# Kernel tuning notes

Measured on AMD Instinct MI355X. Metric: run time of the kernel, lower is better.

Reference implementation:

```python
import jax, jax.numpy as jnp
import numpy as np

B, N, C, H = 32, 4096, 768, 8
DH = C // H

def setup_inputs() -> dict:
    key = jax.random.key(0)
    k1, k2, k3, k4, k5, k6 = jax.random.split(key, 6)
    s = 0.02
    return {
        "x": jax.random.normal(k1, (B, N, C), dtype=jnp.float32),
        "queries": jax.random.normal(k2, (C,), dtype=jnp.float32),
        "Wq": jax.random.normal(k3, (C, C), dtype=jnp.float32) * s,
        "Wkv": jax.random.normal(k4, (2 * C, C), dtype=jnp.float32) * s,
        "Wproj": jax.random.normal(k5, (C, C), dtype=jnp.float32) * s,
        "bproj": jax.random.normal(k6, (C,), dtype=jnp.float32) * s,
    }

def reference(x, queries, Wq, Wkv, Wproj, bproj):
    # q: single learnable query, shared across batch. torch Linear: y = x @ W^T
    q = (queries @ Wq.T).reshape(H, DH)              # [H, DH]
    kv = jnp.einsum('bnc,ec->bne', x, Wkv)           # [B, N, 2C]
    k, v = jnp.split(kv, 2, axis=-1)
    k = k.reshape(B, N, H, DH)
    v = v.reshape(B, N, H, DH)
    # NOTE: original applies no 1/sqrt(d) scaling
    dots = jnp.einsum('hd,bnhd->bhn', q, k)          # [B, H, N]
    attn = jax.nn.softmax(dots, axis=-1)
    out = jnp.einsum('bhn,bnhd->bhd', attn, v)       # [B, H, DH]
    out = out.reshape(B, 1, C)
    out = jnp.einsum('bnc,ec->bne', out, Wproj) + bproj
    return out                                        # [B, 1, C]
```

## Files before the change

kernel.cpp:

```cpp
#include <hip/hip_runtime.h>

#define B_ 32
#define N_ 4096
#define C_ 768
#define H_ 8
#define DH_ 96
#define TILE 8
#define ROWS 256
#define NT (ROWS / TILE)
#define NCH (N_ / ROWS)
#define TFL (TILE * C_)
#define NDG 4

struct F3 { float x, y, z; };

#define BARL() do { asm volatile("s_waitcnt lgkmcnt(0)" ::: "memory"); \
                    __builtin_amdgcn_s_barrier(); } while (0)

__global__ __launch_bounds__(256) void k_prep(const float* __restrict__ queries,
    const float* __restrict__ Wq, const float* __restrict__ Wkv,
    float* __restrict__ wqep) {
  __shared__ float qh[24];
  const int h = blockIdx.x, dg = blockIdx.y;
  const int tid = threadIdx.x, lane = tid & 63, wv = tid >> 6;
  const int d0 = dg * 24;

  float4 q0 = *(const float4*)(queries + lane * 4);
  float4 q1 = *(const float4*)(queries + 256 + lane * 4);
  float4 q2 = *(const float4*)(queries + 512 + lane * 4);
#pragma unroll
  for (int j = 0; j < 6; ++j) {
    int dl = wv * 6 + j;
    const float* wr = Wq + (size_t)(h * DH_ + d0 + dl) * C_ + lane * 4;
    float4 w0 = *(const float4*)(wr);
    float4 w1 = *(const float4*)(wr + 256);
    float4 w2 = *(const float4*)(wr + 512);
    float a = w0.x * q0.x;
    a = fmaf(w0.y, q0.y, a); a = fmaf(w0.z, q0.z, a); a = fmaf(w0.w, q0.w, a);
    a = fmaf(w1.x, q1.x, a); a = fmaf(w1.y, q1.y, a);
    a = fmaf(w1.z, q1.z, a); a = fmaf(w1.w, q1.w, a);
    a = fmaf(w2.x, q2.x, a); a = fmaf(w2.y, q2.y, a);
    a = fmaf(w2.z, q2.z, a); a = fmaf(w2.w, q2.w, a);
#pragma unroll
    for (int off = 32; off; off >>= 1) a += __shfl_xor(a, off);
    if (lane == 0) qh[dl] = a;
  }
  __syncthreads();

  const int c0 = tid * 3;
  const float* base = Wkv + (size_t)(h * DH_ + d0) * C_ + c0;
  float a0 = 0.f, a1 = 0.f, a2 = 0.f;
#pragma unroll 8
  for (int d = 0; d < 24; ++d) {
    float qd = qh[d];
    const float* p = base + (size_t)d * C_;
    a0 = fmaf(qd, p[0], a0);
    a1 = fmaf(qd, p[1], a1);
    a2 = fmaf(qd, p[2], a2);
  }
  float* o = wqep + ((size_t)dg * H_ + h) * C_ + c0;
  o[0] = a0; o[1] = a1; o[2] = a2;
}

__global__ __attribute__((amdgpu_flat_work_group_size(256, 256),
                          amdgpu_waves_per_eu(2, 2))) void k_fused(
    const float* __restrict__ x, const float* __restrict__ wqep,
    float* __restrict__ part, float* __restrict__ sout) {
  extern __shared__ __align__(16) float xdyn[];
  __shared__ __align__(16) float wlds[2][TILE][H_];
  __shared__ float sden[4][4];

  const int ch = blockIdx.x, b = blockIdx.y;
  const int tid = threadIdx.x, lane = tid & 63, wid = tid >> 6;
  const int rbase = (wid & 1) * 4;
  const int hbase = (wid >> 1) * 4;
  const int col = lane * 4;
  const float* xc = x + ((size_t)b * N_ + (size_t)ch * ROWS) * C_;

  float4 wqv[4][3];
#pragma unroll
  for (int h = 0; h < 4; ++h)
#pragma unroll
    for (int p = 0; p < 3; ++p) {
      float4 s = *(const float4*)(wqep + (size_t)(hbase + h) * C_ + p * 256 + col);
#pragma unroll
      for (int dg = 1; dg < NDG; ++dg) {
        float4 v = *(const float4*)(wqep + ((size_t)dg * H_ + hbase + h) * C_ + p * 256 + col);
        s.x += v.x; s.y += v.y; s.z += v.z; s.w += v.w;
      }
      wqv[h][p] = s;
    }

  float acc[H_][3];
#pragma unroll
  for (int h = 0; h < H_; ++h) { acc[h][0] = 0.f; acc[h][1] = 0.f; acc[h][2] = 0.f; }
  float sreg = 0.f;

#define STAGE(BI, T) do {                                                      \
    const float* gt_ = xc + (size_t)(T) * TFL;                                 \
    float* bn_ = xdyn + (size_t)(BI) * TFL;                                    \
    _Pragma("unroll")                                                          \
    for (int j = 0; j < 6; ++j) {                                              \
      int k = wid * 6 + j;                                                     \
      __builtin_amdgcn_global_load_lds(                                        \
        (const __attribute__((address_space(1))) void*)(gt_ + k * 256 + lane * 4), \
        (__attribute__((address_space(3))) void*)(bn_ + k * 256),              \
        16, 0, 0);                                                             \
    }                                                                          \
  } while (0)

#define PHASEC(XB, PC) do {                                                    \
    const int c0 = tid * 3;                                                    \
    _Pragma("unroll")                                                          \
    for (int r = 0; r < TILE; ++r) {                                           \
      float4 wA = *(const float4*)(&wlds[PC][r][0]);                           \
      float4 wB = *(const float4*)(&wlds[PC][r][4]);                           \
      F3 xv = *(const F3*)((XB) + (size_t)r * C_ + c0);                        \
      acc[0][0] = fmaf(wA.x, xv.x, acc[0][0]);                                 \
      acc[0][1] = fmaf(wA.x, xv.y, acc[0][1]);                                 \
      acc[0][2] = fmaf(wA.x, xv.z, acc[0][2]);                                 \
      acc[1][0] = fmaf(wA.y, xv.x, acc[1][0]);                                 \
      acc[1][1] = fmaf(wA.y, xv.y, acc[1][1]);                                 \
      acc[1][2] = fmaf(wA.y, xv.z, acc[1][2]);                                 \
      acc[2][0] = fmaf(wA.z, xv.x, acc[2][0]);                                 \
      acc[2][1] = fmaf(wA.z, xv.y, acc[2][1]);                                 \
      acc[2][2] = fmaf(wA.z, xv.z, acc[2][2]);                                 \
      acc[3][0] = fmaf(wA.w, xv.x, acc[3][0]);                                 \
      acc[3][1] = fmaf(wA.w, xv.y, acc[3][1]);                                 \
      acc[3][2] = fmaf(wA.w, xv.z, acc[3][2]);                                 \
      acc[4][0] = fmaf(wB.x, xv.x, acc[4][0]);                                 \
      acc[4][1] = fmaf(wB.x, xv.y, acc[4][1]);                                 \
      acc[4][2] = fmaf(wB.x, xv.z, acc[4][2]);                                 \
      acc[5][0] = fmaf(wB.y, xv.x, acc[5][0]);                                 \
      acc[5][1] = fmaf(wB.y, xv.y, acc[5][1]);                                 \
      acc[5][2] = fmaf(wB.y, xv.z, acc[5][2]);                                 \
      acc[6][0] = fmaf(wB.z, xv.x, acc[6][0]);                                 \
      acc[6][1] = fmaf(wB.z, xv.y, acc[6][1]);                                 \
      acc[6][2] = fmaf(wB.z, xv.z, acc[6][2]);                                 \
      acc[7][0] = fmaf(wB.w, xv.x, acc[7][0]);                                 \
      acc[7][1] = fmaf(wB.w, xv.y, acc[7][1]);                                 \
      acc[7][2] = fmaf(wB.w, xv.z, acc[7][2]);                                 \
    }                                                                          \
  } while (0)

  STAGE(0, 0);

  int bi = 0;
  for (int t = 0; t < NT; ++t) {
    BARL();
    if (t + 1 < NT) { int nb = bi + 1; if (nb >= 3) nb -= 3; STAGE(nb, t + 1); }

    if (t > 0) {
      int pb = bi + 2; if (pb >= 3) pb -= 3;
      PHASEC(xdyn + (size_t)pb * TFL, (t & 1) ^ 1);
    }

    if (t + 1 < NT) { asm volatile("s_waitcnt vmcnt(6)" ::: "memory"); }
    else            { asm volatile("s_waitcnt vmcnt(0)" ::: "memory"); }

    const float* xb = xdyn + (size_t)bi * TFL;
    const int P = t & 1;

#pragma unroll
    for (int rr = 0; rr < 4; ++rr) {
      const int r = rbase + rr;
      const float* xr = xb + r * C_ + col;
      float4 xv0 = *(const float4*)(xr);
      float4 xv1 = *(const float4*)(xr + 256);
      float4 xv2 = *(const float4*)(xr + 512);
      float d[4];
#pragma unroll
      for (int h = 0; h < 4; ++h) {
        float a = xv0.x * wqv[h][0].x;
        a = fmaf(xv0.y, wqv[h][0].y, a);
        a = fmaf(xv0.z, wqv[h][0].z, a);
        a = fmaf(xv0.w, wqv[h][0].w, a);
        a = fmaf(xv1.x, wqv[h][1].x, a);
        a = fmaf(xv1.y, wqv[h][1].y, a);
        a = fmaf(xv1.z, wqv[h][1].z, a);
        a = fmaf(xv1.w, wqv[h][1].w, a);
        a = fmaf(xv2.x, wqv[h][2].x, a);
        a = fmaf(xv2.y, wqv[h][2].y, a);
        a = fmaf(xv2.z, wqv[h][2].z, a);
        a = fmaf(xv2.w, wqv[h][2].w, a);
        d[h] = a;
      }
      const int s1 = lane & 1, s2 = lane & 2;
      float A0 = (s1 ? d[1] : d[0]) + __shfl_xor(s1 ? d[0] : d[1], 1);
      float A1 = (s1 ? d[3] : d[2]) + __shfl_xor(s1 ? d[2] : d[3], 1);
      float Q  = (s2 ? A1 : A0) + __shfl_xor(s2 ? A0 : A1, 2);
      Q += __shfl_xor(Q, 4);
      Q += __shfl_xor(Q, 8);
      Q += __shfl_xor(Q, 16);
      Q += __shfl_xor(Q, 32);
      float w = __expf(Q - 20.f);
      if (lane < 4) { wlds[P][r][hbase + lane] = w; sreg += w; }
    }
    ++bi; if (bi >= 3) bi -= 3;
  }

  BARL();
  {
    int pb = bi + 2; if (pb >= 3) pb -= 3;
    PHASEC(xdyn + (size_t)pb * TFL, (NT - 1) & 1);
  }

  {
    const int c0 = tid * 3;
    float* pp = part + ((size_t)(b * NCH + ch) * H_) * C_ + c0;
#pragma unroll
    for (int h = 0; h < H_; ++h) {
      F3 o = { acc[h][0], acc[h][1], acc[h][2] };
      *(F3*)(pp + (size_t)h * C_) = o;
    }
    if (lane < 4) sden[wid][lane] = sreg;
    BARL();
    if (tid < H_) {
      int hh = tid >> 2;
      float den = sden[2 * hh][tid & 3] + sden[2 * hh + 1][tid & 3];
      sout[(size_t)(b * NCH + ch) * H_ + tid] = den;
    }
  }
#undef PHASEC
#undef STAGE
}

__global__ __launch_bounds__(256) void k_combout(
    const float* __restrict__ part, const float* __restrict__ spart,
    const float* __restrict__ Wkv, float* __restrict__ out1) {
  __shared__ __align__(16) float xb[C_];
  const int h = blockIdx.x, b = blockIdx.y;
  const int tid = threadIdx.x, lane = tid & 63, wv = tid >> 6;

  const float* sp = spart + (size_t)b * NCH * H_ + h;
  float den = 0.f;
#pragma unroll
  for (int ch = 0; ch < NCH; ++ch) den += sp[(size_t)ch * H_];
  const float inv = 1.f / den;

  const int c0 = tid * 3;
  const float* pp = part + ((size_t)(b * NCH) * H_ + h) * C_ + c0;
  float a0 = 0.f, a1 = 0.f, a2 = 0.f;
#pragma unroll
  for (int ch = 0; ch < NCH; ++ch) {
    const float* p = pp + (size_t)ch * H_ * C_;
    a0 += p[0]; a1 += p[1]; a2 += p[2];
  }
  xb[c0] = a0 * inv; xb[c0 + 1] = a1 * inv; xb[c0 + 2] = a2 * inv;
  __syncthreads();

  float4 x0 = *(const float4*)(&xb[lane * 4]);
  float4 x1 = *(const float4*)(&xb[256 + lane * 4]);
  float4 x2 = *(const float4*)(&xb[512 + lane * 4]);
#pragma unroll 4
  for (int j = 0; j < 24; ++j) {
    int e = h * DH_ + wv * 24 + j;
    const float* wr = Wkv + (size_t)(C_ + e) * C_ + lane * 4;
    float4 w0 = *(const float4*)(wr);
    float4 w1 = *(const float4*)(wr + 256);
    float4 w2 = *(const float4*)(wr + 512);
    float a = w0.x * x0.x;
    a = fmaf(w0.y, x0.y, a); a = fmaf(w0.z, x0.z, a); a = fmaf(w0.w, x0.w, a);
    a = fmaf(w1.x, x1.x, a); a = fmaf(w1.y, x1.y, a);
    a = fmaf(w1.z, x1.z, a); a = fmaf(w1.w, x1.w, a);
    a = fmaf(w2.x, x2.x, a); a = fmaf(w2.y, x2.y, a);
    a = fmaf(w2.z, x2.z, a); a = fmaf(w2.w, x2.w, a);
#pragma unroll
    for (int off = 32; off; off >>= 1) a += __shfl_xor(a, off);
    if (lane == 0) out1[(size_t)b * C_ + e] = a;
  }
}

__global__ __launch_bounds__(256) void k_proj2(
    const float* __restrict__ out1, const float* __restrict__ Wproj,
    const float* __restrict__ bproj, float* __restrict__ y) {
  __shared__ __align__(16) float xb[C_];
  const int esl = blockIdx.x, b = blockIdx.y;
  const int tid = threadIdx.x, lane = tid & 63, wv = tid >> 6;

  if (tid < 192) ((float4*)xb)[tid] = ((const float4*)(out1 + (size_t)b * C_))[tid];
  __syncthreads();

  float4 x0 = *(const float4*)(&xb[lane * 4]);
  float4 x1 = *(const float4*)(&xb[256 + lane * 4]);
  float4 x2 = *(const float4*)(&xb[512 + lane * 4]);
#pragma unroll 4
  for (int j = 0; j < 24; ++j) {
    int e = esl * DH_ + wv * 24 + j;
    const float* wr = Wproj + (size_t)e * C_ + lane * 4;
    float4 w0 = *(const float4*)(wr);
    float4 w1 = *(const float4*)(wr + 256);
    float4 w2 = *(const float4*)(wr + 512);
    float a = w0.x * x0.x;
    a = fmaf(w0.y, x0.y, a); a = fmaf(w0.z, x0.z, a); a = fmaf(w0.w, x0.w, a);
    a = fmaf(w1.x, x1.x, a); a = fmaf(w1.y, x1.y, a);
    a = fmaf(w1.z, x1.z, a); a = fmaf(w1.w, x1.w, a);
    a = fmaf(w2.x, x2.x, a); a = fmaf(w2.y, x2.y, a);
    a = fmaf(w2.z, x2.z, a); a = fmaf(w2.w, x2.w, a);
#pragma unroll
    for (int off = 32; off; off >>= 1) a += __shfl_xor(a, off);
    if (lane == 0) y[(size_t)b * C_ + e] = a + bproj[e];
  }
}

extern "C" void kernel_launch(void* const* d_in, const int* in_sizes, int n_in,
                              void* d_out, int out_size, void* d_ws, size_t ws_size,
                              hipStream_t stream) {
  const float* x       = (const float*)d_in[0];
  const float* queries = (const float*)d_in[1];
  const float* Wq      = (const float*)d_in[2];
  const float* Wkv     = (const float*)d_in[3];
  const float* Wproj   = (const float*)d_in[4];
  const float* bproj   = (const float*)d_in[5];
  float* y  = (float*)d_out;
  float* ws = (float*)d_ws;

  float* wqep  = ws;
  float* spart = ws + 24576;
  float* part  = ws + 32768;
  float* out1  = part + (size_t)B_ * NCH * H_ * C_;

  hipLaunchKernelGGL(k_prep,    dim3(H_, NDG),  dim3(256), 0, stream, queries, Wq, Wkv, wqep);
  hipLaunchKernelGGL(k_fused,   dim3(NCH, B_),  dim3(256),
                     3 * TFL * sizeof(float), stream, x, wqep, part, spart);
  hipLaunchKernelGGL(k_combout, dim3(H_, B_),   dim3(256), 0, stream, part, spart, Wkv, out1);
  hipLaunchKernelGGL(k_proj2,   dim3(H_, B_),   dim3(256), 0, stream, out1, Wproj, bproj, y);
}
```

Measured before the change: 158.9 us.

## Double k_fused block size to 512 threads, splitting heads across thread halves

Grows the fused attention block from 256 to 512 threads. Each wave now scores 2 rows instead of 4, and the weighted-accumulate phase gives each half of the block 4 heads instead of all 8, halving per-thread accumulators and staging loads. The aim is more waves in flight to hide the latency of streaming x and to lower register pressure. The cost is more threads contending on LDS and a wider barrier, and launch bounds now request 4 blocks per CU, which the LDS budget may not allow.

```diff
diff --git a/kernel.cpp b/kernel.cpp
--- a/kernel.cpp
+++ b/kernel.cpp
@@ -62,19 +62,20 @@
   o[0] = a0; o[1] = a1; o[2] = a2;
 }
 
-__global__ __attribute__((amdgpu_flat_work_group_size(256, 256),
-                          amdgpu_waves_per_eu(2, 2))) void k_fused(
+__global__ __launch_bounds__(512, 4) void k_fused(
     const float* __restrict__ x, const float* __restrict__ wqep,
     float* __restrict__ part, float* __restrict__ sout) {
   extern __shared__ __align__(16) float xdyn[];
   __shared__ __align__(16) float wlds[2][TILE][H_];
-  __shared__ float sden[4][4];
+  __shared__ float sden[8][4];
 
   const int ch = blockIdx.x, b = blockIdx.y;
   const int tid = threadIdx.x, lane = tid & 63, wid = tid >> 6;
-  const int rbase = (wid & 1) * 4;
-  const int hbase = (wid >> 1) * 4;
+  const int rbase = (wid & 3) * 2;
+  const int hbase = (wid >> 2) * 4;
   const int col = lane * 4;
+  const int chh = tid >> 8;
+  const int cc0 = (tid & 255) * 3;
   const float* xc = x + ((size_t)b * N_ + (size_t)ch * ROWS) * C_;
 
   float4 wqv[4][3];
@@ -91,17 +92,17 @@
       wqv[h][p] = s;
     }
 
-  float acc[H_][3];
-#pragma unroll
-  for (int h = 0; h < H_; ++h) { acc[h][0] = 0.f; acc[h][1] = 0.f; acc[h][2] = 0.f; }
+  float acc[4][3];
+#pragma unroll
+  for (int h = 0; h < 4; ++h) { acc[h][0] = 0.f; acc[h][1] = 0.f; acc[h][2] = 0.f; }
   float sreg = 0.f;
 
 #define STAGE(BI, T) do {                                                      \
     const float* gt_ = xc + (size_t)(T) * TFL;                                 \
     float* bn_ = xdyn + (size_t)(BI) * TFL;                                    \
     _Pragma("unroll")                                                          \
-    for (int j = 0; j < 6; ++j) {                                              \
-      int k = wid * 6 + j;                                                     \
+    for (int j = 0; j < 3; ++j) {                                              \
+      int k = wid * 3 + j;                                                     \
       __builtin_amdgcn_global_load_lds(                                        \
         (const __attribute__((address_space(1))) void*)(gt_ + k * 256 + lane * 4), \
         (__attribute__((address_space(3))) void*)(bn_ + k * 256),              \
@@ -110,36 +111,23 @@
   } while (0)
 
 #define PHASEC(XB, PC) do {                                                    \
-    const int c0 = tid * 3;                                                    \
+    const float* wp_ = &wlds[PC][0][chh * 4];                                  \
     _Pragma("unroll")                                                          \
     for (int r = 0; r < TILE; ++r) {                                           \
-      float4 wA = *(const float4*)(&wlds[PC][r][0]);                           \
-      float4 wB = *(const float4*)(&wlds[PC][r][4]);                           \
-      F3 xv = *(const F3*)((XB) + (size_t)r * C_ + c0);                        \
-      acc[0][0] = fmaf(wA.x, xv.x, acc[0][0]);                                 \
-      acc[0][1] = fmaf(wA.x, xv.y, acc[0][1]);                                 \
-      acc[0][2] = fmaf(wA.x, xv.z, acc[0][2]);                                 \
-      acc[1][0] = fmaf(wA.y, xv.x, acc[1][0]);                                 \
-      acc[1][1] = fmaf(wA.y, xv.y, acc[1][1]);                                 \
-      acc[1][2] = fmaf(wA.y, xv.z, acc[1][2]);                                 \
-      acc[2][0] = fmaf(wA.z, xv.x, acc[2][0]);                                 \
-      acc[2][1] = fmaf(wA.z, xv.y, acc[2][1]);                                 \
-      acc[2][2] = fmaf(wA.z, xv.z, acc[2][2]);                                 \
-      acc[3][0] = fmaf(wA.w, xv.x, acc[3][0]);                                 \
-      acc[3][1] = fmaf(wA.w, xv.y, acc[3][1]);                                 \
-      acc[3][2] = fmaf(wA.w, xv.z, acc[3][2]);                                 \
-      acc[4][0] = fmaf(wB.x, xv.x, acc[4][0]);                                 \
-      acc[4][1] = fmaf(wB.x, xv.y, acc[4][1]);                                 \
-      acc[4][2] = fmaf(wB.x, xv.z, acc[4][2]);                                 \
-      acc[5][0] = fmaf(wB.y, xv.x, acc[5][0]);                                 \
-      acc[5][1] = fmaf(wB.y, xv.y, acc[5][1]);                                 \
-      acc[5][2] = fmaf(wB.y, xv.z, acc[5][2]);                                 \
-      acc[6][0] = fmaf(wB.z, xv.x, acc[6][0]);                                 \
-      acc[6][1] = fmaf(wB.z, xv.y, acc[6][1]);                                 \
-      acc[6][2] = fmaf(wB.z, xv.z, acc[6][2]);                                 \
-      acc[7][0] = fmaf(wB.w, xv.x, acc[7][0]);                                 \
-      acc[7][1] = fmaf(wB.w, xv.y, acc[7][1]);                                 \
-      acc[7][2] = fmaf(wB.w, xv.z, acc[7][2]);                                 \
+      float4 wv = *(const float4*)(wp_ + r * H_);      \
+      F3 xv = *(const F3*)((XB) + (size_t)r * C_ + cc0);                       \
+      acc[0][0] = fmaf(wv.x, xv.x, acc[0][0]);                                 \
+      acc[0][1] = fmaf(wv.x, xv.y, acc[0][1]);                                 \
+      acc[0][2] = fmaf(wv.x, xv.z, acc[0][2]);                                 \
+      acc[1][0] = fmaf(wv.y, xv.x, acc[1][0]);                                 \
+      acc[1][1] = fmaf(wv.y, xv.y, acc[1][1]);                                 \
+      acc[1][2] = fmaf(wv.y, xv.z, acc[1][2]);                                 \
+      acc[2][0] = fmaf(wv.z, xv.x, acc[2][0]);                                 \
+      acc[2][1] = fmaf(wv.z, xv.y, acc[2][1]);                                 \
+      acc[2][2] = fmaf(wv.z, xv.z, acc[2][2]);                                 \
+      acc[3][0] = fmaf(wv.w, xv.x, acc[3][0]);                                 \
+      acc[3][1] = fmaf(wv.w, xv.y, acc[3][1]);                                 \
+      acc[3][2] = fmaf(wv.w, xv.z, acc[3][2]);                                 \
     }                                                                          \
   } while (0)
 
@@ -155,14 +143,14 @@
       PHASEC(xdyn + (size_t)pb * TFL, (t & 1) ^ 1);
     }
 
-    if (t + 1 < NT) { asm volatile("s_waitcnt vmcnt(6)" ::: "memory"); }
+    if (t + 1 < NT) { asm volatile("s_waitcnt vmcnt(3)" ::: "memory"); }
     else            { asm volatile("s_waitcnt vmcnt(0)" ::: "memory"); }
 
     const float* xb = xdyn + (size_t)bi * TFL;
     const int P = t & 1;
 
 #pragma unroll
-    for (int rr = 0; rr < 4; ++rr) {
+    for (int rr = 0; rr < 2; ++rr) {
       const int r = rbase + rr;
       const float* xr = xb + r * C_ + col;
       float4 xv0 = *(const float4*)(xr);
@@ -206,18 +194,18 @@
   }
 
   {
-    const int c0 = tid * 3;
-    float* pp = part + ((size_t)(b * NCH + ch) * H_) * C_ + c0;
-#pragma unroll
-    for (int h = 0; h < H_; ++h) {
+    float* pp = part + ((size_t)(b * NCH + ch) * H_ + chh * 4) * C_ + cc0;
+#pragma unroll
+    for (int h = 0; h < 4; ++h) {
       F3 o = { acc[h][0], acc[h][1], acc[h][2] };
       *(F3*)(pp + (size_t)h * C_) = o;
     }
     if (lane < 4) sden[wid][lane] = sreg;
     BARL();
     if (tid < H_) {
-      int hh = tid >> 2;
-      float den = sden[2 * hh][tid & 3] + sden[2 * hh + 1][tid & 3];
+      int g = (tid >> 2) * 4;
+      float den = sden[g][tid & 3] + sden[g + 1][tid & 3]
+                + sden[g + 2][tid & 3] + sden[g + 3][tid & 3];
       sout[(size_t)(b * NCH + ch) * H_ + tid] = den;
     }
   }
@@ -321,7 +309,7 @@
   float* out1  = part + (size_t)B_ * NCH * H_ * C_;
 
   hipLaunchKernelGGL(k_prep,    dim3(H_, NDG),  dim3(256), 0, stream, queries, Wq, Wkv, wqep);
-  hipLaunchKernelGGL(k_fused,   dim3(NCH, B_),  dim3(256),
+  hipLaunchKernelGGL(k_fused,   dim3(NCH, B_),  dim3(512),
                      3 * TFL * sizeof(float), stream, x, wqep, part, spart);
   hipLaunchKernelGGL(k_combout, dim3(H_, B_),   dim3(256), 0, stream, part, spart, Wkv, out1);
   hipLaunchKernelGGL(k_proj2,   dim3(H_, B_),   dim3(256), 0, stream, out1, Wproj, bproj, y);
```

After: 350.0 us. +120.3%, slower.
